# Performance work log

Hardware: AMD Instinct MI355X
Metric: run time of the kernel (lower is better)

The kernel has to match this reference:

```python
import jax, jax.numpy as jnp
import numpy as np

N = 100000

def gcn_conv(x, edge_index, W, b):
    # PyG GCNConv: y = D^-1/2 (A + I) D^-1/2 (x W) + b
    xw = x @ W  # [N, F_out]
    row, col = edge_index[0], edge_index[1]
    # add self loops
    loops = jnp.arange(N, dtype=row.dtype)
    row = jnp.concatenate([row, loops])
    col = jnp.concatenate([col, loops])
    ones = jnp.ones(row.shape[0], dtype=xw.dtype)
    deg = jax.ops.segment_sum(ones, row, num_segments=N)
    dinv = jnp.where(deg > 0, jax.lax.rsqrt(deg), 0.0)
    norm = dinv[row] * dinv[col]  # [E+N]
    msgs = norm[:, None] * xw[col]  # gather + scale
    out = jax.ops.segment_sum(msgs, row, num_segments=N)  # scatter-add
    return out + b

def setup_inputs() -> dict:
    key = jax.random.key(0)
    ks = jax.random.split(key, 10)
    E = 3200000
    return {
        "x": jax.random.normal(ks[0], (N, 256), dtype=jnp.float32),
        "edge_index": jax.random.randint(ks[1], (2, E), 0, N, dtype=jnp.int64),
        "W1": jax.random.normal(ks[2], (256, 256), dtype=jnp.float32) * 0.0625,
        "b1": jnp.zeros((256,), dtype=jnp.float32),
        "W2": jax.random.normal(ks[3], (256, 128), dtype=jnp.float32) * 0.0625,
        "b2": jnp.zeros((128,), dtype=jnp.float32),
        "Wmu": jax.random.normal(ks[4], (128, 128), dtype=jnp.float32) * 0.088,
        "bmu": jnp.zeros((128,), dtype=jnp.float32),
        "Wlv": jax.random.normal(ks[5], (128, 128), dtype=jnp.float32) * 0.088,
        "blv": jnp.zeros((128,), dtype=jnp.float32),
    }

def reference(x, edge_index, W1, b1, W2, b2, Wmu, bmu, Wlv, blv):
    z = gcn_conv(x, edge_index, W1, b1)
    z = jax.nn.relu(z)
    z = gcn_conv(z, edge_index, W2, b2)
    mu = z @ Wmu + bmu
    logvar = z @ Wlv + blv
    return (mu, logvar)
```

## Files before the change

kernel.cpp:

```cpp
#include <hip/hip_runtime.h>

typedef unsigned int uint;
typedef unsigned short ushort;

#define NNODES 100000
#define MP 100096
#define NP 100096

typedef __attribute__((ext_vector_type(8))) short bf16x8;
typedef __attribute__((ext_vector_type(4))) float f32x4;

__device__ __forceinline__ float b2f(uint u) {
    union { float f; uint i; } x; x.i = u << 16; return x.f;
}
__device__ __forceinline__ ushort f2b(float f) {
    uint u = __float_as_uint(f);
    u = (u + 0x7fffu + ((u >> 16) & 1u)) >> 16;
    return (ushort)u;
}


__global__ void count_edges(const int* __restrict__ rows, int* __restrict__ cnt, int E) {
    int i = blockIdx.x * 256 + threadIdx.x;
    if (i < E) {
        uint r = (uint)rows[i];
        if (r < NNODES) atomicAdd(&cnt[r], 1);
    }
}

__global__ __launch_bounds__(256) void dinv_rowstart(
        const int* __restrict__ cnt, float* __restrict__ dinv,
        int* __restrict__ row_start, int* __restrict__ gcur) {
    int i = blockIdx.x * 256 + threadIdx.x;
    int lane = threadIdx.x & 63;
    int c = (i < NNODES) ? cnt[i] : 0;
    if (i < NNODES) dinv[i] = rsqrtf((float)(c + 1));
    int incl = c;
#pragma unroll
    for (int off = 1; off < 64; off <<= 1) {
        int u = __shfl_up(incl, off, 64);
        if (lane >= off) incl += u;
    }
    int base = 0;
    if (lane == 63) base = atomicAdd(gcur, incl);
    base = __shfl(base, 63, 64);
    if (i < NNODES) row_start[i] = base + incl - c;
}

__global__ void fill_csr(const int* __restrict__ rows, const int* __restrict__ cols,
                         const int* __restrict__ row_start, int* __restrict__ cursor,
                         int* __restrict__ csr_col, int E) {
    int i = blockIdx.x * 256 + threadIdx.x;
    if (i < E) {
        uint r = (uint)rows[i];
        uint c = (uint)cols[i];
        if (r < NNODES && c < NNODES) {
            int slot = atomicAdd(&cursor[r], 1);
            csr_col[row_start[r] + slot] = (int)c;
        }
    }
}


__global__ void convert_x(const float* __restrict__ X, ushort* __restrict__ Xb, int n4) {
    int i = blockIdx.x * 256 + threadIdx.x;
    if (i < n4) {
        float4 v = ((const float4*)X)[i];
        uint2 o;
        o.x = (uint)f2b(v.x) | ((uint)f2b(v.y) << 16);
        o.y = (uint)f2b(v.z) | ((uint)f2b(v.w) << 16);
        ((uint2*)Xb)[i] = o;
    }
}

__global__ void transpose_w(const float* __restrict__ W, ushort* __restrict__ Wt, int K, int Nout) {
    int i = blockIdx.x * 256 + threadIdx.x;
    if (i < K * Nout) {
        int k = i / Nout, n = i % Nout;
        Wt[(size_t)n * K + k] = f2b(W[i]);
    }
}

__global__ void concat_bias(const float* __restrict__ a, const float* __restrict__ b,
                            float* __restrict__ o) {
    int i = threadIdx.x;
    o[i] = (i < 128) ? a[i] : b[i - 128];
}


template<int KDIM, int NOUT, int EPI>
__global__ __launch_bounds__(256, 2) void gemm_bt(
        const ushort* __restrict__ A, const ushort* __restrict__ Bt,
        ushort* __restrict__ Cb, float* __restrict__ Cf,
        const float* __restrict__ dinv, const float* __restrict__ bias, int Mvalid) {
    __shared__ __align__(16) ushort Alds[128][72];
    __shared__ __align__(16) ushort Blds[128][72];
    __shared__ float dlds[128];

    const int tid = threadIdx.x;
    const int bm0 = blockIdx.x * 128;
    const int bn0 = blockIdx.y * 128;
    const int w = tid >> 6, lane = tid & 63;
    const int wm = (w >> 1) * 64, wn = (w & 1) * 64;
    const int lm = lane & 15, lq = lane >> 4;

    f32x4 acc[4][4] = {};
    if (EPI == 0 && tid < 128) dlds[tid] = dinv[bm0 + tid];

    const int sr = tid >> 3;
    const int sc = (tid & 7) * 8;

    for (int k0 = 0; k0 < KDIM; k0 += 64) {
        uint4 ar[4], br[4];
#pragma unroll
        for (int i = 0; i < 4; ++i) {
            int r = sr + i * 32;
            ar[i] = *(const uint4*)&A[(size_t)(bm0 + r) * KDIM + k0 + sc];
            br[i] = *(const uint4*)&Bt[(size_t)(bn0 + r) * KDIM + k0 + sc];
        }
        __syncthreads();
#pragma unroll
        for (int i = 0; i < 4; ++i) {
            int r = sr + i * 32;
            *(uint4*)&Alds[r][sc] = ar[i];
            *(uint4*)&Blds[r][sc] = br[i];
        }
        __syncthreads();
#pragma unroll
        for (int kk = 0; kk < 64; kk += 32) {
            bf16x8 af[4], bfr[4];
#pragma unroll
            for (int t = 0; t < 4; ++t) af[t]  = *(const bf16x8*)&Alds[wm + t * 16 + lm][kk + lq * 8];
#pragma unroll
            for (int t = 0; t < 4; ++t) bfr[t] = *(const bf16x8*)&Blds[wn + t * 16 + lm][kk + lq * 8];
#pragma unroll
            for (int tm = 0; tm < 4; ++tm)
#pragma unroll
                for (int tn = 0; tn < 4; ++tn)
                    acc[tm][tn] = __builtin_amdgcn_mfma_f32_16x16x32_bf16(
                        af[tm], bfr[tn], acc[tm][tn], 0, 0, 0);
        }
    }

#pragma unroll
    for (int tm = 0; tm < 4; ++tm) {
#pragma unroll
        for (int tn = 0; tn < 4; ++tn) {
#pragma unroll
            for (int r = 0; r < 4; ++r) {
                int lr = wm + tm * 16 + lq * 4 + r;
                int gr = bm0 + lr;
                int gc = bn0 + wn + tn * 16 + lm;
                float v = acc[tm][tn][r];
                if (EPI == 0) {
                    v *= dlds[lr];
                    Cb[(size_t)gr * NOUT + gc] = f2b(v);
                } else {
                    v += bias[gc];
                    if (gr < Mvalid) {
                        size_t off = (gc < 128)
                            ? ((size_t)gr * 128 + gc)
                            : ((size_t)NNODES * 128 + (size_t)gr * 128 + (gc - 128));
                        Cf[off] = v;
                    }
                }
            }
        }
    }
}


template<int F, bool RELU>
__global__ __launch_bounds__(256) void aggregate(
        const ushort* __restrict__ xw, const int* __restrict__ csr_col,
        const int* __restrict__ row_start, const int* __restrict__ cnt,
        const float* __restrict__ dinv, const float* __restrict__ bias,
        ushort* __restrict__ out) {
    const int row = blockIdx.x * 4 + (threadIdx.x >> 6);
    if (row >= NNODES) return;
    const int lane = threadIdx.x & 63;
    const int s = row_start[row];
    const int e = s + cnt[row];
    const float d = dinv[row];

    if (F == 256) {
        const int f0 = lane * 4;
        const ushort* base = xw + f0;
        uint2 sv = *(const uint2*)(base + (size_t)row * F);
        float a0 = b2f(sv.x & 0xffffu), a1 = b2f(sv.x >> 16);
        float a2 = b2f(sv.y & 0xffffu), a3 = b2f(sv.y >> 16);
        int i = s;
        for (; i + 8 <= e; i += 8) {
            int c[8];
            uint2 v[8];
#pragma unroll
            for (int j = 0; j < 8; ++j) c[j] = csr_col[i + j];
#pragma unroll
            for (int j = 0; j < 8; ++j) v[j] = *(const uint2*)(base + (size_t)c[j] * F);
#pragma unroll
            for (int j = 0; j < 8; ++j) {
                a0 += b2f(v[j].x & 0xffffu); a1 += b2f(v[j].x >> 16);
                a2 += b2f(v[j].y & 0xffffu); a3 += b2f(v[j].y >> 16);
            }
        }
        for (; i < e; ++i) {
            uint2 v = *(const uint2*)(base + (size_t)csr_col[i] * F);
            a0 += b2f(v.x & 0xffffu); a1 += b2f(v.x >> 16);
            a2 += b2f(v.y & 0xffffu); a3 += b2f(v.y >> 16);
        }
        float r0 = a0 * d + bias[f0 + 0];
        float r1 = a1 * d + bias[f0 + 1];
        float r2 = a2 * d + bias[f0 + 2];
        float r3 = a3 * d + bias[f0 + 3];
        if (RELU) {
            r0 = fmaxf(r0, 0.f); r1 = fmaxf(r1, 0.f);
            r2 = fmaxf(r2, 0.f); r3 = fmaxf(r3, 0.f);
        }
        uint2 o;
        o.x = (uint)f2b(r0) | ((uint)f2b(r1) << 16);
        o.y = (uint)f2b(r2) | ((uint)f2b(r3) << 16);
        *(uint2*)(out + (size_t)row * F + f0) = o;
    } else {
        const int f0 = lane * 2;
        const ushort* base = xw + f0;
        uint sv = *(const uint*)(base + (size_t)row * F);
        float a0 = b2f(sv & 0xffffu), a1 = b2f(sv >> 16);
        int i = s;
        for (; i + 8 <= e; i += 8) {
            int c[8];
            uint v[8];
#pragma unroll
            for (int j = 0; j < 8; ++j) c[j] = csr_col[i + j];
#pragma unroll
            for (int j = 0; j < 8; ++j) v[j] = *(const uint*)(base + (size_t)c[j] * F);
#pragma unroll
            for (int j = 0; j < 8; ++j) {
                a0 += b2f(v[j] & 0xffffu); a1 += b2f(v[j] >> 16);
            }
        }
        for (; i < e; ++i) {
            uint v = *(const uint*)(base + (size_t)csr_col[i] * F);
            a0 += b2f(v & 0xffffu); a1 += b2f(v >> 16);
        }
        float r0 = a0 * d + bias[f0 + 0];
        float r1 = a1 * d + bias[f0 + 1];
        if (RELU) { r0 = fmaxf(r0, 0.f); r1 = fmaxf(r1, 0.f); }
        *(uint*)(out + (size_t)row * F + f0) = (uint)f2b(r0) | ((uint)f2b(r1) << 16);
    }
}


extern "C" void kernel_launch(void* const* d_in, const int* in_sizes, int n_in,
                              void* d_out, int out_size, void* d_ws, size_t ws_size,
                              hipStream_t stream) {
    (void)n_in; (void)out_size; (void)ws_size;
    const float* x   = (const float*)d_in[0];
    const int*   ei  = (const int*)d_in[1];
    const float* W1  = (const float*)d_in[2];
    const float* b1  = (const float*)d_in[3];
    const float* W2  = (const float*)d_in[4];
    const float* b2  = (const float*)d_in[5];
    const float* Wmu = (const float*)d_in[6];
    const float* bmu = (const float*)d_in[7];
    const float* Wlv = (const float*)d_in[8];
    const float* blv = (const float*)d_in[9];
    float* out = (float*)d_out;

    const int E = in_sizes[1] / 2;
    const int* rows = ei;
    const int* cols = ei + E;

    char* ws = (char*)d_ws;
    size_t o = 0;
    int*   cnt       = (int*)(ws + o); o += (size_t)NP * 4;
    int*   cursor    = (int*)(ws + o); o += (size_t)NP * 4;
    int*   gcur      = (int*)(ws + o); o += 256;
    const size_t ZBYTES = o;
    int*   row_start = (int*)(ws + o); o += (size_t)NP * 4;
    float* dinv      = (float*)(ws + o); o += (size_t)NP * 4;
    float* bcat      = (float*)(ws + o); o += 256 * 4;
    int*   csr       = (int*)(ws + o); o += (size_t)E * 4;
    ushort* W1t      = (ushort*)(ws + o); o += 256 * 256 * 2;
    ushort* W2t      = (ushort*)(ws + o); o += 256 * 128 * 2;
    ushort* Wht      = (ushort*)(ws + o); o += 256 * 128 * 2;
    o = (o + 4095) & ~(size_t)4095;
    ushort* bufA = (ushort*)(ws + o); o += (size_t)MP * 256 * 2;
    ushort* bufB = (ushort*)(ws + o); o += (size_t)MP * 256 * 2;

    ushort* xb  = bufA;
    ushort* xw1 = bufB;
    ushort* z1  = bufA;
    ushort* xw2 = bufB;
    ushort* z2  = bufA;

    hipMemsetAsync(d_ws, 0, ZBYTES, stream);

    count_edges<<<dim3((E + 255) / 256), 256, 0, stream>>>(rows, cnt, E);
    dinv_rowstart<<<dim3((NNODES + 255) / 256), 256, 0, stream>>>(cnt, dinv, row_start, gcur);
    fill_csr<<<dim3((E + 255) / 256), 256, 0, stream>>>(rows, cols, row_start, cursor, csr, E);

    convert_x<<<dim3((NNODES * 256 / 4 + 255) / 256), 256, 0, stream>>>(x, xb, NNODES * 256 / 4);
    transpose_w<<<dim3((256 * 256 + 255) / 256), 256, 0, stream>>>(W1, W1t, 256, 256);
    transpose_w<<<dim3((256 * 128 + 255) / 256), 256, 0, stream>>>(W2, W2t, 256, 128);
    transpose_w<<<dim3((128 * 128 + 255) / 256), 256, 0, stream>>>(Wmu, Wht, 128, 128);
    transpose_w<<<dim3((128 * 128 + 255) / 256), 256, 0, stream>>>(Wlv, Wht + 128 * 128, 128, 128);
    concat_bias<<<1, 256, 0, stream>>>(bmu, blv, bcat);

    gemm_bt<256, 256, 0><<<dim3(MP / 128, 2), 256, 0, stream>>>(xb, W1t, xw1, nullptr, dinv, nullptr, MP);
    aggregate<256, true><<<dim3(NNODES / 4), 256, 0, stream>>>(xw1, csr, row_start, cnt, dinv, b1, z1);

    gemm_bt<256, 128, 0><<<dim3(MP / 128, 1), 256, 0, stream>>>(z1, W2t, xw2, nullptr, dinv, nullptr, MP);
    aggregate<128, false><<<dim3(NNODES / 4), 256, 0, stream>>>(xw2, csr, row_start, cnt, dinv, b2, z2);

    gemm_bt<128, 256, 1><<<dim3(MP / 128, 2), 256, 0, stream>>>(z2, Wht, nullptr, out, dinv, bcat, NNODES);
}
```

Baseline: 1.026 ms.

## Bucket CSR by column range and aggregate rows in column-phased sweeps

CSR construction now sorts each row's edges into 32 column buckets, using a per-row, per-bucket count and cursor array. Aggregation changes so that each wave owns 49 rows held in registers and sweeps the column buckets in lockstep across all resident waves, with a block barrier between phases. The aim is to keep gathers across the GPU confined to one column range at a time, so that slice of the feature table stays cache-resident instead of being fetched at random across the whole table. In exchange it costs many accumulator registers, masked dummy loads for empty buckets, barrier stalls, and serial tails for buckets holding more than two edges.

```diff
diff --git a/kernel.cpp b/kernel.cpp
--- a/kernel.cpp
+++ b/kernel.cpp
@@ -6,6 +6,9 @@
 #define NNODES 100000
 #define MP 100096
 #define NP 100096
+#define NB 32
+#define RPW 49
+#define AGG_BLOCKS 1021
 
 typedef __attribute__((ext_vector_type(8))) short bf16x8;
 typedef __attribute__((ext_vector_type(4))) float f32x4;
@@ -19,23 +22,39 @@
     return (ushort)u;
 }
 
-
-__global__ void count_edges(const int* __restrict__ rows, int* __restrict__ cnt, int E) {
+__device__ __forceinline__ int colbucket(int c) {
+    return (int)(((uint)c * 671u) >> 21);
+}
+
+
+__global__ void count_edges2(const int* __restrict__ rows, const int* __restrict__ cols,
+                             int* __restrict__ cnt2, int E) {
     int i = blockIdx.x * 256 + threadIdx.x;
     if (i < E) {
         uint r = (uint)rows[i];
-        if (r < NNODES) atomicAdd(&cnt[r], 1);
-    }
-}
-
-__global__ __launch_bounds__(256) void dinv_rowstart(
-        const int* __restrict__ cnt, float* __restrict__ dinv,
-        int* __restrict__ row_start, int* __restrict__ gcur) {
-    int i = blockIdx.x * 256 + threadIdx.x;
+        uint c = (uint)cols[i];
+        if (r < NNODES && c < NNODES)
+            atomicAdd(&cnt2[(size_t)r * NB + colbucket((int)c)], 1);
+    }
+}
+
+__global__ __launch_bounds__(256) void scan_rows(
+        const int* __restrict__ cnt2, float* __restrict__ dinv,
+        int2* __restrict__ bb, int* __restrict__ cursor2, int* __restrict__ gcur) {
+    int row = blockIdx.x * 256 + threadIdx.x;
     int lane = threadIdx.x & 63;
-    int c = (i < NNODES) ? cnt[i] : 0;
-    if (i < NNODES) dinv[i] = rsqrtf((float)(c + 1));
-    int incl = c;
+    int c[NB];
+    int deg = 0;
+    if (row < NNODES) {
+#pragma unroll
+        for (int k = 0; k < NB; k += 4) {
+            int4 v = *(const int4*)&cnt2[(size_t)row * NB + k];
+            c[k] = v.x; c[k + 1] = v.y; c[k + 2] = v.z; c[k + 3] = v.w;
+            deg += v.x + v.y + v.z + v.w;
+        }
+        dinv[row] = rsqrtf((float)(deg + 1));
+    }
+    int incl = deg;
 #pragma unroll
     for (int off = 1; off < 64; off <<= 1) {
         int u = __shfl_up(incl, off, 64);
@@ -44,19 +63,26 @@
     int base = 0;
     if (lane == 63) base = atomicAdd(gcur, incl);
     base = __shfl(base, 63, 64);
-    if (i < NNODES) row_start[i] = base + incl - c;
-}
-
-__global__ void fill_csr(const int* __restrict__ rows, const int* __restrict__ cols,
-                         const int* __restrict__ row_start, int* __restrict__ cursor,
-                         int* __restrict__ csr_col, int E) {
+    int p = base + incl - deg;
+    if (row < NNODES) {
+#pragma unroll
+        for (int k = 0; k < NB; ++k) {
+            bb[(size_t)row * NB + k] = make_int2(p, c[k]);
+            cursor2[(size_t)row * NB + k] = p;
+            p += c[k];
+        }
+    }
+}
+
+__global__ void fill_csr2(const int* __restrict__ rows, const int* __restrict__ cols,
+                          int* __restrict__ cursor2, int* __restrict__ csr_col, int E) {
     int i = blockIdx.x * 256 + threadIdx.x;
     if (i < E) {
         uint r = (uint)rows[i];
         uint c = (uint)cols[i];
         if (r < NNODES && c < NNODES) {
-            int slot = atomicAdd(&cursor[r], 1);
-            csr_col[row_start[r] + slot] = (int)c;
+            int pos = atomicAdd(&cursor2[(size_t)r * NB + colbucket((int)c)], 1);
+            csr_col[pos] = (int)c;
         }
     }
 }
@@ -170,82 +196,140 @@
 }
 
 
+template<int F>
+__device__ __forceinline__ void gadd(const ushort* __restrict__ tb, int c, float* a) {
+    if constexpr (F == 256) {
+        uint2 v = *(const uint2*)(tb + (size_t)c * 256);
+        a[0] += b2f(v.x & 0xffffu); a[1] += b2f(v.x >> 16);
+        a[2] += b2f(v.y & 0xffffu); a[3] += b2f(v.y >> 16);
+    } else {
+        uint v = *(const uint*)(tb + (size_t)c * 128);
+        a[0] += b2f(v & 0xffffu); a[1] += b2f(v >> 16);
+    }
+}
+
+template<int F>
+__device__ __forceinline__ void gmask(const ushort* __restrict__ tb, int c, float m, float* a) {
+    if constexpr (F == 256) {
+        uint2 v = *(const uint2*)(tb + (size_t)c * 256);
+        a[0] = fmaf(m, b2f(v.x & 0xffffu), a[0]);
+        a[1] = fmaf(m, b2f(v.x >> 16),     a[1]);
+        a[2] = fmaf(m, b2f(v.y & 0xffffu), a[2]);
+        a[3] = fmaf(m, b2f(v.y >> 16),     a[3]);
+    } else {
+        uint v = *(const uint*)(tb + (size_t)c * 128);
+        a[0] = fmaf(m, b2f(v & 0xffffu), a[0]);
+        a[1] = fmaf(m, b2f(v >> 16),     a[1]);
+    }
+}
+
 template<int F, bool RELU>
-__global__ __launch_bounds__(256) void aggregate(
-        const ushort* __restrict__ xw, const int* __restrict__ csr_col,
-        const int* __restrict__ row_start, const int* __restrict__ cnt,
-        const float* __restrict__ dinv, const float* __restrict__ bias,
-        ushort* __restrict__ out) {
-    const int row = blockIdx.x * 4 + (threadIdx.x >> 6);
-    if (row >= NNODES) return;
+__global__ __launch_bounds__(128, 2) void agg_phased(
+        const ushort* __restrict__ xw, const int* __restrict__ csr,
+        const int2* __restrict__ bb, const float* __restrict__ dinv,
+        const float* __restrict__ bias, ushort* __restrict__ out, int E) {
+    constexpr int PF = F / 64;
     const int lane = threadIdx.x & 63;
-    const int s = row_start[row];
-    const int e = s + cnt[row];
-    const float d = dinv[row];
-
-    if (F == 256) {
-        const int f0 = lane * 4;
-        const ushort* base = xw + f0;
-        uint2 sv = *(const uint2*)(base + (size_t)row * F);
-        float a0 = b2f(sv.x & 0xffffu), a1 = b2f(sv.x >> 16);
-        float a2 = b2f(sv.y & 0xffffu), a3 = b2f(sv.y >> 16);
-        int i = s;
-        for (; i + 8 <= e; i += 8) {
-            int c[8];
-            uint2 v[8];
-#pragma unroll
-            for (int j = 0; j < 8; ++j) c[j] = csr_col[i + j];
-#pragma unroll
-            for (int j = 0; j < 8; ++j) v[j] = *(const uint2*)(base + (size_t)c[j] * F);
-#pragma unroll
-            for (int j = 0; j < 8; ++j) {
-                a0 += b2f(v[j].x & 0xffffu); a1 += b2f(v[j].x >> 16);
-                a2 += b2f(v[j].y & 0xffffu); a3 += b2f(v[j].y >> 16);
+    const int wv = blockIdx.x * 2 + (threadIdx.x >> 6);
+    const int row0 = wv * RPW;
+    const int myrow = row0 + lane;
+    const bool rv = (lane < RPW) && (myrow < NNODES);
+    const float dvl = rv ? dinv[myrow] : 0.f;
+    const int Emax = E - 1;
+    const ushort* tb = xw + lane * PF;
+
+    float a[RPW][PF];
+#pragma unroll
+    for (int r = 0; r < RPW; ++r)
+#pragma unroll
+        for (int k = 0; k < PF; ++k) a[r][k] = 0.f;
+
+#pragma unroll
+    for (int r = 0; r < RPW; ++r) gadd<F>(tb, row0 + r, a[r]);
+
+    int2 sn = rv ? bb[(size_t)myrow * NB + 0] : make_int2(0, 0);
+    int i0 = (sn.x < Emax) ? sn.x : Emax;
+    int i1 = (sn.x + 1 < Emax) ? sn.x + 1 : Emax;
+    int c0v = csr[i0];
+    int c1v = csr[i1];
+
+    for (int b = 0; b < NB; ++b) {
+        const int bn = (b + 1 < NB) ? b + 1 : b;
+        int2 snn = rv ? bb[(size_t)myrow * NB + bn] : make_int2(0, 0);
+        const int dummyc = b * 3125;
+
+#pragma unroll
+        for (int r = 0; r < RPW; ++r) {
+            int n = __shfl(sn.y, r, 64);
+            int cc = __shfl(c0v, r, 64);
+            float m = (n >= 1) ? 1.f : 0.f;
+            cc = (n >= 1) ? cc : dummyc;
+            gmask<F>(tb, cc, m, a[r]);
+        }
+
+        int j0 = (snn.x < Emax) ? snn.x : Emax;
+        int j1 = (snn.x + 1 < Emax) ? snn.x + 1 : Emax;
+        int c0n = csr[j0];
+        int c1n = csr[j1];
+
+#pragma unroll
+        for (int r = 0; r < RPW; ++r) {
+            int n = __shfl(sn.y, r, 64);
+            int cc = __shfl(c1v, r, 64);
+            float m = (n >= 2) ? 1.f : 0.f;
+            cc = (n >= 2) ? cc : dummyc;
+            gmask<F>(tb, cc, m, a[r]);
+        }
+
+#pragma unroll
+        for (int r = 0; r < RPW; ++r) {
+            int n = __shfl(sn.y, r, 64);
+            if (n >= 3) {
+                int s = __shfl(sn.x, r, 64);
+                int e = s + n;
+                for (int i = s + 2; i < e; ++i) gadd<F>(tb, csr[i], a[r]);
             }
         }
-        for (; i < e; ++i) {
-            uint2 v = *(const uint2*)(base + (size_t)csr_col[i] * F);
-            a0 += b2f(v.x & 0xffffu); a1 += b2f(v.x >> 16);
-            a2 += b2f(v.y & 0xffffu); a3 += b2f(v.y >> 16);
-        }
-        float r0 = a0 * d + bias[f0 + 0];
-        float r1 = a1 * d + bias[f0 + 1];
-        float r2 = a2 * d + bias[f0 + 2];
-        float r3 = a3 * d + bias[f0 + 3];
-        if (RELU) {
-            r0 = fmaxf(r0, 0.f); r1 = fmaxf(r1, 0.f);
-            r2 = fmaxf(r2, 0.f); r3 = fmaxf(r3, 0.f);
-        }
-        uint2 o;
-        o.x = (uint)f2b(r0) | ((uint)f2b(r1) << 16);
-        o.y = (uint)f2b(r2) | ((uint)f2b(r3) << 16);
-        *(uint2*)(out + (size_t)row * F + f0) = o;
+
+        sn = snn; c0v = c0n; c1v = c1n;
+        __syncthreads();
+    }
+
+    if constexpr (F == 256) {
+        float4 bv = *(const float4*)&bias[lane * 4];
+#pragma unroll
+        for (int r = 0; r < RPW; ++r) {
+            int row = row0 + r;
+            if (row < NNODES) {
+                float d = __shfl(dvl, r, 64);
+                float r0 = a[r][0] * d + bv.x;
+                float r1 = a[r][1] * d + bv.y;
+                float r2 = a[r][2] * d + bv.z;
+                float r3 = a[r][3] * d + bv.w;
+                if (RELU) {
+                    r0 = fmaxf(r0, 0.f); r1 = fmaxf(r1, 0.f);
+                    r2 = fmaxf(r2, 0.f); r3 = fmaxf(r3, 0.f);
+                }
+                uint2 o;
+                o.x = (uint)f2b(r0) | ((uint)f2b(r1) << 16);
+                o.y = (uint)f2b(r2) | ((uint)f2b(r3) << 16);
+                *(uint2*)(out + (size_t)row * 256 + lane * 4) = o;
+            }
+        }
     } else {
-        const int f0 = lane * 2;
-        const ushort* base = xw + f0;
-        uint sv = *(const uint*)(base + (size_t)row * F);
-        float a0 = b2f(sv & 0xffffu), a1 = b2f(sv >> 16);
-        int i = s;
-        for (; i + 8 <= e; i += 8) {
-            int c[8];
-            uint v[8];
-#pragma unroll
-            for (int j = 0; j < 8; ++j) c[j] = csr_col[i + j];
-#pragma unroll
-            for (int j = 0; j < 8; ++j) v[j] = *(const uint*)(base + (size_t)c[j] * F);
-#pragma unroll
-            for (int j = 0; j < 8; ++j) {
-                a0 += b2f(v[j] & 0xffffu); a1 += b2f(v[j] >> 16);
+        float2 bv = *(const float2*)&bias[lane * 2];
+#pragma unroll
+        for (int r = 0; r < RPW; ++r) {
+            int row = row0 + r;
+            if (row < NNODES) {
+                float d = __shfl(dvl, r, 64);
+                float r0 = a[r][0] * d + bv.x;
+                float r1 = a[r][1] * d + bv.y;
+                if (RELU) { r0 = fmaxf(r0, 0.f); r1 = fmaxf(r1, 0.f); }
+                *(uint*)(out + (size_t)row * 128 + lane * 2) =
+                    (uint)f2b(r0) | ((uint)f2b(r1) << 16);
             }
         }
-        for (; i < e; ++i) {
-            uint v = *(const uint*)(base + (size_t)csr_col[i] * F);
-            a0 += b2f(v & 0xffffu); a1 += b2f(v >> 16);
-        }
-        float r0 = a0 * d + bias[f0 + 0];
-        float r1 = a1 * d + bias[f0 + 1];
-        if (RELU) { r0 = fmaxf(r0, 0.f); r1 = fmaxf(r1, 0.f); }
-        *(uint*)(out + (size_t)row * F + f0) = (uint)f2b(r0) | ((uint)f2b(r1) << 16);
     }
 }
 
@@ -272,20 +356,20 @@
 
     char* ws = (char*)d_ws;
     size_t o = 0;
-    int*   cnt       = (int*)(ws + o); o += (size_t)NP * 4;
-    int*   cursor    = (int*)(ws + o); o += (size_t)NP * 4;
-    int*   gcur      = (int*)(ws + o); o += 256;
-    const size_t ZBYTES = o;
-    int*   row_start = (int*)(ws + o); o += (size_t)NP * 4;
-    float* dinv      = (float*)(ws + o); o += (size_t)NP * 4;
-    float* bcat      = (float*)(ws + o); o += 256 * 4;
-    int*   csr       = (int*)(ws + o); o += (size_t)E * 4;
-    ushort* W1t      = (ushort*)(ws + o); o += 256 * 256 * 2;
-    ushort* W2t      = (ushort*)(ws + o); o += 256 * 128 * 2;
-    ushort* Wht      = (ushort*)(ws + o); o += 256 * 128 * 2;
+    int2*  bb   = (int2*)(ws + o);  o += (size_t)NNODES * NB * sizeof(int2);
+    float* dinv = (float*)(ws + o); o += (size_t)NP * 4;
+    int*   gcur = (int*)(ws + o);   o += 256;
+    float* bcat = (float*)(ws + o); o += 1024;
+    ushort* W1t = (ushort*)(ws + o); o += 256 * 256 * 2;
+    ushort* W2t = (ushort*)(ws + o); o += 256 * 128 * 2;
+    ushort* Wht = (ushort*)(ws + o); o += 256 * 128 * 2;
+    int*   csr  = (int*)(ws + o);   o += (size_t)E * 4;
     o = (o + 4095) & ~(size_t)4095;
     ushort* bufA = (ushort*)(ws + o); o += (size_t)MP * 256 * 2;
     ushort* bufB = (ushort*)(ws + o); o += (size_t)MP * 256 * 2;
+
+    int* cnt2    = (int*)bufB;
+    int* cursor2 = (int*)((char*)bufB + (size_t)NNODES * NB * 4);
 
     ushort* xb  = bufA;
     ushort* xw1 = bufB;
@@ -293,11 +377,12 @@
     ushort* xw2 = bufB;
     ushort* z2  = bufA;
 
-    hipMemsetAsync(d_ws, 0, ZBYTES, stream);
-
-    count_edges<<<dim3((E + 255) / 256), 256, 0, stream>>>(rows, cnt, E);
-    dinv_rowstart<<<dim3((NNODES + 255) / 256), 256, 0, stream>>>(cnt, dinv, row_start, gcur);
-    fill_csr<<<dim3((E + 255) / 256), 256, 0, stream>>>(rows, cols, row_start, cursor, csr, E);
+    (void)hipMemsetAsync(cnt2, 0, (size_t)NNODES * NB * 4, stream);
+    (void)hipMemsetAsync(gcur, 0, 4, stream);
+
+    count_edges2<<<dim3((E + 255) / 256), 256, 0, stream>>>(rows, cols, cnt2, E);
+    scan_rows<<<dim3((NNODES + 255) / 256), 256, 0, stream>>>(cnt2, dinv, bb, cursor2, gcur);
+    fill_csr2<<<dim3((E + 255) / 256), 256, 0, stream>>>(rows, cols, cursor2, csr, E);
 
     convert_x<<<dim3((NNODES * 256 / 4 + 255) / 256), 256, 0, stream>>>(x, xb, NNODES * 256 / 4);
     transpose_w<<<dim3((256 * 256 + 255) / 256), 256, 0, stream>>>(W1, W1t, 256, 256);
@@ -307,10 +392,10 @@
     concat_bias<<<1, 256, 0, stream>>>(bmu, blv, bcat);
 
     gemm_bt<256, 256, 0><<<dim3(MP / 128, 2), 256, 0, stream>>>(xb, W1t, xw1, nullptr, dinv, nullptr, MP);
-    aggregate<256, true><<<dim3(NNODES / 4), 256, 0, stream>>>(xw1, csr, row_start, cnt, dinv, b1, z1);
+    agg_phased<256, true><<<dim3(AGG_BLOCKS), 128, 0, stream>>>(xw1, csr, bb, dinv, b1, z1, E);
 
     gemm_bt<256, 128, 0><<<dim3(MP / 128, 1), 256, 0, stream>>>(z1, W2t, xw2, nullptr, dinv, nullptr, MP);
-    aggregate<128, false><<<dim3(NNODES / 4), 256, 0, stream>>>(xw2, csr, row_start, cnt, dinv, b2, z2);
+    agg_phased<128, false><<<dim3(AGG_BLOCKS), 128, 0, stream>>>(xw2, csr, bb, dinv, b2, z2, E);
 
     gemm_bt<128, 256, 1><<<dim3(MP / 128, 2), 256, 0, stream>>>(z2, Wht, nullptr, out, dinv, bcat, NNODES);
 }
```

New measurement: 3.544 ms. +245.3%, slower.
